# Kernel optimization log

Hardware: AMD Instinct MI355X
Metric: run time of the kernel (lower is better)

The kernel has to match this reference:

```python
import jax, jax.numpy as jnp
import numpy as np

ENC_DIM, DEC_DIM, ATT_DIM = 512, 512, 256
B, T = 64, 4096


def setup_inputs() -> dict:
    key = jax.random.key(0)
    ks = jax.random.split(key, 7)
    s_enc = 1.0 / np.sqrt(ENC_DIM)
    s_dec = 1.0 / np.sqrt(DEC_DIM)
    s_att = 1.0 / np.sqrt(ATT_DIM)
    return {
        "encoder_features": jax.random.normal(ks[0], (B, T, ENC_DIM), jnp.float32),
        "decoder_hidden": jax.random.normal(ks[1], (B, DEC_DIM), jnp.float32),
        # encoder_proj: Linear(encoder_dim, attention_dim) with bias
        "W_enc": jax.random.uniform(ks[2], (ENC_DIM, ATT_DIM), jnp.float32, -s_enc, s_enc),
        "b_enc": jax.random.uniform(ks[3], (ATT_DIM,), jnp.float32, -s_enc, s_enc),
        # decoder_proj: Linear(decoder_dim, attention_dim, bias=False)
        "W_dec": jax.random.uniform(ks[4], (DEC_DIM, ATT_DIM), jnp.float32, -s_dec, s_dec),
        # attention_vector: Linear(attention_dim, 1) with bias
        "v_att": jax.random.uniform(ks[5], (ATT_DIM,), jnp.float32, -s_att, s_att),
        "b_att": jax.random.uniform(ks[6], (), jnp.float32, -s_att, s_att),
    }


def reference(encoder_features, decoder_hidden, W_enc, b_enc, W_dec, v_att, b_att):
    # (B,T,A) = (B,T,E)@(E,A) + b
    enc_proj = jnp.einsum("bte,ea->bta", encoder_features, W_enc) + b_enc
    # (B,1,A)
    dec_proj = (decoder_hidden @ W_dec)[:, None, :]
    energy = jnp.tanh(enc_proj + dec_proj)                      # (B,T,A)
    scores = jnp.einsum("bta,a->bt", energy, v_att) + b_att     # (B,T)
    attention_weights = jax.nn.softmax(scores, axis=1)          # (B,T)
    context = jnp.einsum("bt,bte->be", attention_weights, encoder_features)
    return (context, attention_weights)
```

## Files before the change

### kernel.cpp

```cpp
#include <hip/hip_runtime.h>
#include <hip/hip_bf16.h>

#define E_DIM 512
#define D_DIM 512
#define A_DIM 256
#define B_SZ  64
#define T_SZ  4096
#define TT    32
#define NTB   (T_SZ / TT)
#define TPB   16
#define SLICES (NTB / TPB)
#define LDT   (E_DIM + 8)

typedef __bf16 bf16_t;
typedef bf16_t bf16x8 __attribute__((ext_vector_type(8)));
typedef float  f32x4  __attribute__((ext_vector_type(4)));

__device__ __forceinline__ unsigned short f2bf(float x) {
    union { float f; unsigned int u; } v; v.f = x;
    unsigned int u = v.u;
    return (unsigned short)((u + 0x7FFFu + ((u >> 16) & 1u)) >> 16);
}
__device__ __forceinline__ float bf2f(unsigned short h) {
    union { unsigned int u; float f; } v; v.u = ((unsigned int)h) << 16; return v.f;
}
__device__ __forceinline__ float tanh_fast(float x) {
    x = fminf(8.0f, fmaxf(-8.0f, x));
    float e = __expf(2.0f * x);
    return 1.0f - 2.0f * __builtin_amdgcn_rcpf(e + 1.0f);
}

__global__ __launch_bounds__(256) void prep_kernel(
    const float* __restrict__ dec, const float* __restrict__ W_enc,
    const float* __restrict__ b_enc, const float* __restrict__ W_dec,
    float* __restrict__ dp, unsigned short* __restrict__ Wt,
    float* __restrict__ ctx_acc, float* __restrict__ S)
{
    const int bid = blockIdx.x, tid = threadIdx.x;
    if (bid < B_SZ) {
        float s = b_enc[tid];
        const float* dr = dec + bid * D_DIM;
        #pragma unroll 8
        for (int d = 0; d < D_DIM; ++d)
            s = fmaf(dr[d], W_dec[d * A_DIM + tid], s);
        dp[bid * A_DIM + tid] = s;
        ctx_acc[bid * E_DIM + tid]       = 0.0f;
        ctx_acc[bid * E_DIM + 256 + tid] = 0.0f;
        if (tid == 0) S[bid] = 0.0f;
    } else {
        int base = (bid - B_SZ) * 2048;
        #pragma unroll
        for (int i = 0; i < 8; ++i) {
            int idx = base + tid + i * 256;
            int a = idx >> 9, e = idx & 511;
            Wt[idx] = f2bf(W_enc[e * A_DIM + a]);
        }
    }
}

__global__ __launch_bounds__(512, 4) void attn_main(
    const float* __restrict__ enc, const unsigned short* __restrict__ Wt,
    const float* __restrict__ dpg, const float* __restrict__ vatt,
    float* __restrict__ u_out, float* __restrict__ ctx_acc,
    float* __restrict__ S)
{
    const int p = blockIdx.x;
    const int b = p >> 3, slice = p & 7;
    const int tid = threadIdx.x;

    __shared__ unsigned short tile[2][TT * LDT];
    __shared__ float spart[8][TT];
    __shared__ float uu[TT];
    __shared__ float dp_s[A_DIM];
    __shared__ float vv[A_DIM];

    if (tid < A_DIM) {
        dp_s[tid] = dpg[b * A_DIM + tid];
        vv[tid]   = vatt[tid];
    }

    const int w = tid >> 6, lane = tid & 63;
    const int m16 = lane & 15, q = lane >> 4;

    const float4* src0 = (const float4*)(enc +
        ((size_t)b * T_SZ + (size_t)slice * TPB * TT) * E_DIM);

    float4 r[8];
    #pragma unroll
    for (int it = 0; it < 8; ++it) r[it] = src0[tid + it * 512];
    #pragma unroll
    for (int it = 0; it < 8; ++it) {
        int idx = tid + it * 512;
        int rr = idx >> 7, cc = idx & 127;
        ushort4 h;
        h.x = f2bf(r[it].x); h.y = f2bf(r[it].y);
        h.z = f2bf(r[it].z); h.w = f2bf(r[it].w);
        *(ushort4*)&tile[0][rr * LDT + cc * 4] = h;
    }
    __syncthreads();

    float va0, va1, dv0, dv1;
    {
        int a0 = w * 32 + m16;
        va0 = vv[a0]; va1 = vv[a0 + 16];
        dv0 = dp_s[a0]; dv1 = dp_s[a0 + 16];
    }

    const unsigned short* WtW = Wt + (size_t)(w * 32) * E_DIM;

    float c_acc = 0.0f;
    float sS    = 0.0f;

    for (int i = 0; i < TPB; ++i) {
        const int cur = i & 1, nxt = cur ^ 1;

        if (i + 1 < TPB) {
            const float4* srcn = src0 + (size_t)(i + 1) * 4096;
            #pragma unroll
            for (int it = 0; it < 8; ++it) r[it] = srcn[tid + it * 512];
        }

        f32x4 acc[2][2];
        #pragma unroll
        for (int mi = 0; mi < 2; ++mi)
            #pragma unroll
            for (int ni = 0; ni < 2; ++ni)
                acc[mi][ni] = (f32x4){0.f, 0.f, 0.f, 0.f};

        #pragma unroll 4
        for (int k0 = 0; k0 < E_DIM; k0 += 32) {
            const int ka = k0 + q * 8;
            bf16x8 afr0 = *(const bf16x8*)&tile[cur][(m16) * LDT + ka];
            bf16x8 afr1 = *(const bf16x8*)&tile[cur][(16 + m16) * LDT + ka];
            bf16x8 bfr0 = *(const bf16x8*)&WtW[(m16) * E_DIM + ka];
            bf16x8 bfr1 = *(const bf16x8*)&WtW[(16 + m16) * E_DIM + ka];
            acc[0][0] = __builtin_amdgcn_mfma_f32_16x16x32_bf16(afr0, bfr0, acc[0][0], 0, 0, 0);
            acc[0][1] = __builtin_amdgcn_mfma_f32_16x16x32_bf16(afr0, bfr1, acc[0][1], 0, 0, 0);
            acc[1][0] = __builtin_amdgcn_mfma_f32_16x16x32_bf16(afr1, bfr0, acc[1][0], 0, 0, 0);
            acc[1][1] = __builtin_amdgcn_mfma_f32_16x16x32_bf16(afr1, bfr1, acc[1][1], 0, 0, 0);
        }

        #pragma unroll
        for (int mi = 0; mi < 2; ++mi) {
            #pragma unroll
            for (int rr = 0; rr < 4; ++rr) {
                float pv = va0 * tanh_fast(acc[mi][0][rr] + dv0)
                         + va1 * tanh_fast(acc[mi][1][rr] + dv1);
                pv += __shfl_xor(pv, 1); pv += __shfl_xor(pv, 2);
                pv += __shfl_xor(pv, 4); pv += __shfl_xor(pv, 8);
                if (m16 == 0) spart[w][mi * 16 + q * 4 + rr] = pv;
            }
        }
        __syncthreads();

        if (tid < TT) {
            float s = 0.f;
            #pragma unroll
            for (int w8 = 0; w8 < 8; ++w8) s += spart[w8][tid];
            float e = __expf(s);
            uu[tid] = e;
            sS += e;
            u_out[(size_t)b * T_SZ + (size_t)(slice * TPB + i) * TT + tid] = e;
        }
        __syncthreads();

        #pragma unroll 8
        for (int t = 0; t < TT; ++t)
            c_acc = fmaf(uu[t], bf2f(tile[cur][t * LDT + tid]), c_acc);

        if (i + 1 < TPB) {
            #pragma unroll
            for (int it = 0; it < 8; ++it) {
                int idx = tid + it * 512;
                int rr = idx >> 7, cc = idx & 127;
                ushort4 h;
                h.x = f2bf(r[it].x); h.y = f2bf(r[it].y);
                h.z = f2bf(r[it].z); h.w = f2bf(r[it].w);
                *(ushort4*)&tile[nxt][rr * LDT + cc * 4] = h;
            }
        }
        __syncthreads();
    }

    atomicAdd(&ctx_acc[(size_t)b * E_DIM + tid], c_acc);
    if (w == 0) {
        sS += __shfl_xor(sS, 1);  sS += __shfl_xor(sS, 2);
        sS += __shfl_xor(sS, 4);  sS += __shfl_xor(sS, 8);
        sS += __shfl_xor(sS, 16); sS += __shfl_xor(sS, 32);
        if (lane == 0) atomicAdd(&S[b], sS);
    }
}

__global__ __launch_bounds__(256) void finalize_kernel(
    const float* __restrict__ u, const float* __restrict__ ctx_acc,
    const float* __restrict__ S, float* __restrict__ out)
{
    const int b = blockIdx.x, j = blockIdx.y, tid = threadIdx.x;
    const float invS = 1.0f / S[b];
    const float* ub = u + (size_t)b * T_SZ + j * 1024;
    float* wout = out + B_SZ * E_DIM + (size_t)b * T_SZ + j * 1024;
    #pragma unroll
    for (int it = 0; it < 4; ++it)
        wout[tid + it * 256] = ub[tid + it * 256] * invS;
    if (j == 0) {
        out[(size_t)b * E_DIM + tid]       = ctx_acc[b * E_DIM + tid] * invS;
        out[(size_t)b * E_DIM + 256 + tid] = ctx_acc[b * E_DIM + 256 + tid] * invS;
    }
}

extern "C" void kernel_launch(void* const* d_in, const int* in_sizes, int n_in,
                              void* d_out, int out_size, void* d_ws, size_t ws_size,
                              hipStream_t stream) {
    const float* enc   = (const float*)d_in[0];
    const float* dec   = (const float*)d_in[1];
    const float* W_enc = (const float*)d_in[2];
    const float* b_enc = (const float*)d_in[3];
    const float* W_dec = (const float*)d_in[4];
    const float* v_att = (const float*)d_in[5];
    float* out = (float*)d_out;

    char* ws = (char*)d_ws;
    unsigned short* Wt = (unsigned short*)(ws);
    float* dp          = (float*)(ws + 262144);
    float* u           = (float*)(ws + 327680);
    float* ctx_acc     = (float*)(ws + 1376256);
    float* S           = (float*)(ws + 1507328);

    prep_kernel<<<128, 256, 0, stream>>>(dec, W_enc, b_enc, W_dec, dp, Wt, ctx_acc, S);
    attn_main<<<B_SZ * SLICES, 512, 0, stream>>>(enc, Wt, dp, v_att, u, ctx_acc, S);
    finalize_kernel<<<dim3(B_SZ, 4), 256, 0, stream>>>(u, ctx_acc, S, out);
}
```

Baseline: 893.6 us.

## Keep W_enc fragments in registers and deepen encoder prefetch to two tiles

Each warp now loads its W_enc B-fragments once into registers (32 bf16x8 vectors) instead of reloading them from global memory on every k-step of every tile. The prefetch goes from one tile ahead to two, using two alternating register buffers with a manually unrolled ping-pong loop, so more global loads are in flight during compute. The launch bound is relaxed from 4 to 2 waves per SIMD to make room for the much larger register footprint. This lowers occupancy and risks spills in exchange for hiding more load latency and removing redundant weight fetches.

```diff
diff --git a/kernel.cpp b/kernel.cpp
--- a/kernel.cpp
+++ b/kernel.cpp
@@ -58,7 +58,69 @@
     }
 }
 
-__global__ __launch_bounds__(512, 4) void attn_main(
+#define LOADT(R, it_) do {                                                    \
+    const float4* s_ = src0 + (size_t)(it_) * 4096;                           \
+    _Pragma("unroll")                                                         \
+    for (int j_ = 0; j_ < 8; ++j_) R[j_] = s_[tid + j_ * 512];                \
+} while (0)
+
+#define DRAINT(R, dst) do {                                                   \
+    _Pragma("unroll")                                                         \
+    for (int j_ = 0; j_ < 8; ++j_) {                                          \
+        int idx_ = tid + j_ * 512;                                            \
+        int rr_ = idx_ >> 7, cc_ = idx_ & 127;                                \
+        ushort4 h_;                                                           \
+        h_.x = f2bf(R[j_].x); h_.y = f2bf(R[j_].y);                           \
+        h_.z = f2bf(R[j_].z); h_.w = f2bf(R[j_].w);                           \
+        *(ushort4*)&(dst)[rr_ * LDT + cc_ * 4] = h_;                          \
+    }                                                                         \
+} while (0)
+
+#define BODY(I, RFREE, RHELD, CUR)  do {                                      \
+    f32x4 a00 = z4, a01 = z4, a10 = z4, a11 = z4;                             \
+    _Pragma("unroll")                                                         \
+    for (int ks = 0; ks < 16; ++ks) {                                         \
+        const int ka = ks * 32 + q * 8;                                       \
+        bf16x8 af0 = *(const bf16x8*)&tile[CUR][m16 * LDT + ka];              \
+        bf16x8 af1 = *(const bf16x8*)&tile[CUR][(16 + m16) * LDT + ka];       \
+        a00 = __builtin_amdgcn_mfma_f32_16x16x32_bf16(af0, breg0[ks], a00, 0, 0, 0); \
+        a01 = __builtin_amdgcn_mfma_f32_16x16x32_bf16(af0, breg1[ks], a01, 0, 0, 0); \
+        a10 = __builtin_amdgcn_mfma_f32_16x16x32_bf16(af1, breg0[ks], a10, 0, 0, 0); \
+        a11 = __builtin_amdgcn_mfma_f32_16x16x32_bf16(af1, breg1[ks], a11, 0, 0, 0); \
+    }                                                                         \
+    _Pragma("unroll")                                                         \
+    for (int rr = 0; rr < 4; ++rr) {                                          \
+        float p0 = va0 * tanh_fast(a00[rr] + dv0)                             \
+                 + va1 * tanh_fast(a01[rr] + dv1);                            \
+        p0 += __shfl_xor(p0, 1); p0 += __shfl_xor(p0, 2);                     \
+        p0 += __shfl_xor(p0, 4); p0 += __shfl_xor(p0, 8);                     \
+        if (m16 == 0) spart[w][q * 4 + rr] = p0;                              \
+        float p1 = va0 * tanh_fast(a10[rr] + dv0)                             \
+                 + va1 * tanh_fast(a11[rr] + dv1);                            \
+        p1 += __shfl_xor(p1, 1); p1 += __shfl_xor(p1, 2);                     \
+        p1 += __shfl_xor(p1, 4); p1 += __shfl_xor(p1, 8);                     \
+        if (m16 == 0) spart[w][16 + q * 4 + rr] = p1;                         \
+    }                                                                         \
+    __syncthreads();                                      \
+    if (tid < TT) {                                                           \
+        float s_ = 0.f;                                                       \
+        _Pragma("unroll")                                                     \
+        for (int w8 = 0; w8 < 8; ++w8) s_ += spart[w8][tid];                  \
+        float e_ = __expf(s_);                                                \
+        uu[tid] = e_;                                                         \
+        sS += e_;                                                             \
+        u_out[(size_t)b * T_SZ + (size_t)(slice * TPB + (I)) * TT + tid] = e_;\
+    }                                                                         \
+    __syncthreads();                                         \
+    if ((I) + 2 < TPB) LOADT(RFREE, (I) + 2);                                 \
+    _Pragma("unroll 8")                                                       \
+    for (int t = 0; t < TT; ++t)                                              \
+        c_acc = fmaf(uu[t], bf2f(tile[CUR][t * LDT + tid]), c_acc);           \
+    if ((I) + 1 < TPB) DRAINT(RHELD, tile[(CUR) ^ 1]);                        \
+    __syncthreads();                                   \
+} while (0)
+
+__global__ __launch_bounds__(512, 2) void attn_main(
     const float* __restrict__ enc, const unsigned short* __restrict__ Wt,
     const float* __restrict__ dpg, const float* __restrict__ vatt,
     float* __restrict__ u_out, float* __restrict__ ctx_acc,
@@ -81,22 +143,23 @@
 
     const int w = tid >> 6, lane = tid & 63;
     const int m16 = lane & 15, q = lane >> 4;
+    const f32x4 z4 = (f32x4){0.f, 0.f, 0.f, 0.f};
+
+    const unsigned short* WtW = Wt + (size_t)(w * 32) * E_DIM;
+    bf16x8 breg0[16], breg1[16];
+    #pragma unroll
+    for (int ks = 0; ks < 16; ++ks) {
+        breg0[ks] = *(const bf16x8*)&WtW[m16 * E_DIM + ks * 32 + q * 8];
+        breg1[ks] = *(const bf16x8*)&WtW[(16 + m16) * E_DIM + ks * 32 + q * 8];
+    }
 
     const float4* src0 = (const float4*)(enc +
         ((size_t)b * T_SZ + (size_t)slice * TPB * TT) * E_DIM);
 
-    float4 r[8];
-    #pragma unroll
-    for (int it = 0; it < 8; ++it) r[it] = src0[tid + it * 512];
-    #pragma unroll
-    for (int it = 0; it < 8; ++it) {
-        int idx = tid + it * 512;
-        int rr = idx >> 7, cc = idx & 127;
-        ushort4 h;
-        h.x = f2bf(r[it].x); h.y = f2bf(r[it].y);
-        h.z = f2bf(r[it].z); h.w = f2bf(r[it].w);
-        *(ushort4*)&tile[0][rr * LDT + cc * 4] = h;
-    }
+    float4 rA[8], rB[8];
+    LOADT(rA, 0);
+    LOADT(rB, 1);
+    DRAINT(rA, tile[0]);
     __syncthreads();
 
     float va0, va1, dv0, dv1;
@@ -106,80 +169,13 @@
         dv0 = dp_s[a0]; dv1 = dp_s[a0 + 16];
     }
 
-    const unsigned short* WtW = Wt + (size_t)(w * 32) * E_DIM;
-
     float c_acc = 0.0f;
     float sS    = 0.0f;
 
-    for (int i = 0; i < TPB; ++i) {
-        const int cur = i & 1, nxt = cur ^ 1;
-
-        if (i + 1 < TPB) {
-            const float4* srcn = src0 + (size_t)(i + 1) * 4096;
-            #pragma unroll
-            for (int it = 0; it < 8; ++it) r[it] = srcn[tid + it * 512];
-        }
-
-        f32x4 acc[2][2];
-        #pragma unroll
-        for (int mi = 0; mi < 2; ++mi)
-            #pragma unroll
-            for (int ni = 0; ni < 2; ++ni)
-                acc[mi][ni] = (f32x4){0.f, 0.f, 0.f, 0.f};
-
-        #pragma unroll 4
-        for (int k0 = 0; k0 < E_DIM; k0 += 32) {
-            const int ka = k0 + q * 8;
-            bf16x8 afr0 = *(const bf16x8*)&tile[cur][(m16) * LDT + ka];
-            bf16x8 afr1 = *(const bf16x8*)&tile[cur][(16 + m16) * LDT + ka];
-            bf16x8 bfr0 = *(const bf16x8*)&WtW[(m16) * E_DIM + ka];
-            bf16x8 bfr1 = *(const bf16x8*)&WtW[(16 + m16) * E_DIM + ka];
-            acc[0][0] = __builtin_amdgcn_mfma_f32_16x16x32_bf16(afr0, bfr0, acc[0][0], 0, 0, 0);
-            acc[0][1] = __builtin_amdgcn_mfma_f32_16x16x32_bf16(afr0, bfr1, acc[0][1], 0, 0, 0);
-            acc[1][0] = __builtin_amdgcn_mfma_f32_16x16x32_bf16(afr1, bfr0, acc[1][0], 0, 0, 0);
-            acc[1][1] = __builtin_amdgcn_mfma_f32_16x16x32_bf16(afr1, bfr1, acc[1][1], 0, 0, 0);
-        }
-
-        #pragma unroll
-        for (int mi = 0; mi < 2; ++mi) {
-            #pragma unroll
-            for (int rr = 0; rr < 4; ++rr) {
-                float pv = va0 * tanh_fast(acc[mi][0][rr] + dv0)
-                         + va1 * tanh_fast(acc[mi][1][rr] + dv1);
-                pv += __shfl_xor(pv, 1); pv += __shfl_xor(pv, 2);
-                pv += __shfl_xor(pv, 4); pv += __shfl_xor(pv, 8);
-                if (m16 == 0) spart[w][mi * 16 + q * 4 + rr] = pv;
-            }
-        }
-        __syncthreads();
-
-        if (tid < TT) {
-            float s = 0.f;
-            #pragma unroll
-            for (int w8 = 0; w8 < 8; ++w8) s += spart[w8][tid];
-            float e = __expf(s);
-            uu[tid] = e;
-            sS += e;
-            u_out[(size_t)b * T_SZ + (size_t)(slice * TPB + i) * TT + tid] = e;
-        }
-        __syncthreads();
-
-        #pragma unroll 8
-        for (int t = 0; t < TT; ++t)
-            c_acc = fmaf(uu[t], bf2f(tile[cur][t * LDT + tid]), c_acc);
-
-        if (i + 1 < TPB) {
-            #pragma unroll
-            for (int it = 0; it < 8; ++it) {
-                int idx = tid + it * 512;
-                int rr = idx >> 7, cc = idx & 127;
-                ushort4 h;
-                h.x = f2bf(r[it].x); h.y = f2bf(r[it].y);
-                h.z = f2bf(r[it].z); h.w = f2bf(r[it].w);
-                *(ushort4*)&tile[nxt][rr * LDT + cc * 4] = h;
-            }
-        }
-        __syncthreads();
+    #pragma unroll 1
+    for (int i2 = 0; i2 < TPB; i2 += 2) {
+        BODY(i2,     rA, rB, 0);
+        BODY(i2 + 1, rB, rA, 1);
     }
 
     atomicAdd(&ctx_acc[(size_t)b * E_DIM + tid], c_acc);
```

After: 762.8 us. 14.6% less time.
